# Kernel tuning notes

Hardware: AMD Instinct MI355X
Metric: run time of the kernel (lower is better)

The kernel has to match this reference:

```python
import jax, jax.numpy as jnp
import numpy as np

EPS = 1e-5
N_CAMERAS, N_POINTS = 6, 4


def _bilinear_sample(feats, gx, gy):
    # feats: [B, C, H, W]; gx, gy: [B, Q] in [-1, 1]; align_corners=False, zero padding
    B, C, H, W = feats.shape
    ix = ((gx + 1.0) * W - 1.0) * 0.5
    iy = ((gy + 1.0) * H - 1.0) * 0.5
    x0 = jnp.floor(ix)
    y0 = jnp.floor(iy)
    fx = ix - x0
    fy = iy - y0
    x0i = x0.astype(jnp.int32)
    y0i = y0.astype(jnp.int32)
    ff = feats.reshape(B, C, H * W)

    def corner(xi, yi, w):
        valid = (xi >= 0) & (xi < W) & (yi >= 0) & (yi < H)
        idx = jnp.clip(yi, 0, H - 1) * W + jnp.clip(xi, 0, W - 1)
        v = jnp.take_along_axis(ff, idx[:, None, :], axis=2)  # [B, C, Q]
        return v * (w * valid)[:, None, :]

    return (corner(x0i, y0i, (1 - fx) * (1 - fy))
            + corner(x0i + 1, y0i, fx * (1 - fy))
            + corner(x0i, y0i + 1, (1 - fx) * fy)
            + corner(x0i + 1, y0i + 1, fx * fy))


def setup_inputs() -> dict:
    key = jax.random.key(0)
    ks = jax.random.split(key, 8)
    Hb = Wb = 128
    nq = Hb * Wb
    bs, hidden, N, P = 2, 256, N_CAMERAS, N_POINTS
    C, Hf, Wf = 256, 28, 50

    rho = jnp.broadcast_to((jnp.arange(Hb, dtype=jnp.float32) / Hb)[:, None], (Hb, Wb))
    phi = jnp.broadcast_to((jnp.arange(Wb, dtype=jnp.float32) / Wb)[None, :], (Hb, Wb))
    pc_range = jnp.array([51.2, 2.0 * np.pi, -5.0, 3.0], jnp.float32)
    intervals = jnp.array([51.2 / Hb, 2.0 * np.pi / Wb], jnp.float32)
    img_size = jnp.array([1600.0, 900.0], jnp.float32)

    # realistic pinhole lidar->image matrices for 6 surround cameras
    K = np.array([[1200.0, 0, 800, 0], [0, 1200.0, 450, 0], [0, 0, 1, 0], [0, 0, 0, 1]], np.float32)
    mats = []
    for i in range(N):
        yaw = 2.0 * np.pi * i / N
        c, s = np.cos(yaw), np.sin(yaw)
        R = np.array([[s, -c, 0], [0, 0, -1], [c, s, 0]], np.float32)  # x_right, y_down, z_forward
        E = np.eye(4, dtype=np.float32)
        E[:3, :3] = R
        E[:3, 3] = np.array([0.0, 1.5, 0.5], np.float32)
        mats.append(K @ E)
    lidar2imgs = jnp.asarray(np.broadcast_to(np.stack(mats), (bs, N, 4, 4)).copy())

    return {
        'query': jax.random.normal(ks[0], (nq, bs, hidden), jnp.float32),
        'query_pos': jax.random.normal(ks[1], (nq, bs, hidden), jnp.float32),
        'rho': rho,
        'phi': phi,
        'zz_cord': jax.random.uniform(ks[2], (bs, nq, 1), jnp.float32),
        'img_feats': jax.random.normal(ks[3], (bs, N, C, Hf, Wf), jnp.float32),
        'lidar2imgs': lidar2imgs,
        'intervals': intervals,
        'pc_range': pc_range,
        'img_size': img_size,
        'Wa': jax.random.normal(ks[4], (hidden, N * P), jnp.float32) * 0.02,
        'ba': jnp.zeros((N * P,), jnp.float32),
        'Wo': jax.random.normal(ks[5], (hidden, hidden), jnp.float32) * 0.02,
        'bo': jnp.zeros((hidden,), jnp.float32),
    }


def reference(query, query_pos, rho, phi, zz_cord, img_feats, lidar2imgs,
              intervals, pc_range, img_size, Wa, ba, Wo, bo):
    q = jnp.transpose(query + query_pos, (1, 0, 2))  # [bs, nq, h]
    bs, nq, _ = q.shape
    aw = (q @ Wa + ba).reshape(bs, 1, nq, N_CAMERAS, N_POINTS)

    # polar BEV -> cartesian lidar coords
    r = rho.reshape(-1, 1) * pc_range[0] + intervals[0] / 2  # [nq, 1]
    p = phi.reshape(-1, 1) * pc_range[1] - jnp.pi + intervals[1] / 2
    xx = r * jnp.cos(p)
    yy = r * jnp.sin(p)
    zz = zz_cord * (pc_range[3] - pc_range[2]) + pc_range[2]  # [bs, nq, 1]
    xyz = jnp.concatenate([
        jnp.broadcast_to(xx[None], (bs, nq, 1)),
        jnp.broadcast_to(yy[None], (bs, nq, 1)),
        zz,
        jnp.ones((bs, nq, 1), q.dtype),
    ], axis=-1)  # [bs, nq, 4]

    cam = jnp.einsum('bnij,bqj->bnqi', lidar2imgs, xyz)  # [bs, N, nq, 4]
    zc = cam[..., 2]
    gx = cam[..., 0] / jnp.maximum(zc, EPS) / img_size[0]
    gy = cam[..., 1] / jnp.maximum(zc, EPS) / img_size[1]
    gx = (gx - 0.5) * 2.0
    gy = (gy - 0.5) * 2.0
    mask = (zc > EPS) & (gx > -1.0) & (gx < 1.0) & (gy > -1.0) & (gy < 1.0)  # [bs, N, nq]

    B, N, C, H, W = img_feats.shape
    sampled = _bilinear_sample(img_feats.reshape(B * N, C, H, W),
                               gx.reshape(B * N, nq), gy.reshape(B * N, nq))
    sampled = jnp.nan_to_num(sampled.reshape(B, N, C, nq).transpose(0, 2, 3, 1))  # [bs, C, nq, N]

    maskf = mask.transpose(0, 2, 1)[:, None, :, :, None].astype(q.dtype)  # [bs,1,nq,N,1]
    ws = (jax.nn.sigmoid(aw) * maskf).sum(-1)  # [bs, 1, nq, N]
    out = jnp.einsum('bcqn,bqn->bcq', sampled, ws[:, 0])  # [bs, C, nq]
    out = out.transpose(2, 0, 1) @ Wo + bo + query  # dropout p=0 -> identity
    mask_out = mask.transpose(0, 2, 1)[:, None, :, :, None]  # [bs,1,nq,N,1] bool
    return out, mask_out
```

## Files before the change

kernel.cpp:

```cpp
#include <hip/hip_runtime.h>
#include <math.h>

#define NQ    16384
#define BS    2
#define HID   256
#define NCAM  6
#define NPTS  4
#define CF    256
#define HF    28
#define WF    50
#define HWF   (HF*WF)
#define NIMG  (BS*NCAM)
#define EPSV  1e-5f
#define GQ    16

typedef __attribute__((ext_vector_type(8))) short short8v;
typedef __attribute__((ext_vector_type(4))) float float4v;

__device__ __forceinline__ unsigned short f2bf(float f) {
    unsigned u = __float_as_uint(f);
    u += 0x7fffu + ((u >> 16) & 1u);
    return (unsigned short)(u >> 16);
}
__device__ __forceinline__ float bfLO(unsigned u) { return __uint_as_float(u << 16); }
__device__ __forceinline__ float bfHI(unsigned u) { return __uint_as_float(u & 0xffff0000u); }

__global__ __launch_bounds__(256) void transpose_feats(
    const float* __restrict__ feats, unsigned short* __restrict__ featsT)
{
    __shared__ float tile[32][33];
    const int img = blockIdx.x / 44;
    const int hw0 = (blockIdx.x % 44) * 32;
    const int tx = threadIdx.x & 31;
    const int ty = threadIdx.x >> 5;
    for (int ct = 0; ct < 8; ++ct) {
        const int c0 = ct * 32;
        #pragma unroll
        for (int i = 0; i < 4; ++i) {
            const int c  = c0 + ty + 8 * i;
            const int hw = hw0 + tx;
            tile[ty + 8 * i][tx] = (hw < HWF) ? feats[((size_t)img * CF + c) * HWF + hw] : 0.f;
        }
        __syncthreads();
        #pragma unroll
        for (int i = 0; i < 4; ++i) {
            const int hw = hw0 + ty + 8 * i;
            if (hw < HWF)
                featsT[((size_t)img * HWF + hw) * CF + c0 + tx] = f2bf(tile[tx][ty + 8 * i]);
        }
        __syncthreads();
    }
}

__global__ __launch_bounds__(256) void transpose_wo_wa(
    const float* __restrict__ Wo, const float* __restrict__ Wa,
    unsigned short* __restrict__ WoT, unsigned short* __restrict__ WaT)
{
    if (blockIdx.x < 64) {
        __shared__ float tile[32][33];
        const int kt = blockIdx.x >> 3, nt = blockIdx.x & 7;
        const int tx = threadIdx.x & 31;
        const int ty = threadIdx.x >> 5;
        #pragma unroll
        for (int i = 0; i < 4; ++i)
            tile[ty + 8 * i][tx] = Wo[(size_t)(kt * 32 + ty + 8 * i) * HID + nt * 32 + tx];
        __syncthreads();
        #pragma unroll
        for (int i = 0; i < 4; ++i)
            WoT[(size_t)(nt * 32 + ty + 8 * i) * HID + kt * 32 + tx] = f2bf(tile[tx][ty + 8 * i]);
    } else {
        #pragma unroll
        for (int v = 0; v < 4; ++v) {
            const int idx = (blockIdx.x - 64) * 1024 + v * 256 + threadIdx.x;
            const int j = idx >> 8, k = idx & 255;
            WaT[idx] = (j < 24) ? f2bf(Wa[k * 24 + j]) : (unsigned short)0;
        }
    }
}

__global__ __launch_bounds__(512) void ca_fused3(
    const float* __restrict__ query, const float* __restrict__ query_pos,
    const float* __restrict__ rho,   const float* __restrict__ phi,
    const float* __restrict__ zz,    const unsigned short* __restrict__ featsT,
    const float* __restrict__ l2i,   const float* __restrict__ intervals,
    const float* __restrict__ pc_range, const float* __restrict__ img_size,
    const unsigned short* __restrict__ WaT, const float* __restrict__ ba,
    const unsigned short* __restrict__ WoT, const float* __restrict__ bo,
    float* __restrict__ out)
{
    __shared__ char  fab[GQ * 512];
    __shared__ float awl[GQ][36];

    const int tid  = threadIdx.x;
    const int wave = tid >> 6;
    const int lane = tid & 63;
    const int l32  = lane & 31;
    const int r    = wave * 2 + (lane >> 5);
    const int base = blockIdx.x * GQ;
    const int g    = base + r;
    const int b    = g >> 14;
    const int q    = g & (NQ - 1);
    const size_t qrow = ((size_t)q * BS + b) * HID;

    {
        const float4 a0 = *reinterpret_cast<const float4*>(&query[qrow + 8 * l32]);
        const float4 a1 = *reinterpret_cast<const float4*>(&query[qrow + 8 * l32 + 4]);
        const float4 p0 = *reinterpret_cast<const float4*>(&query_pos[qrow + 8 * l32]);
        const float4 p1 = *reinterpret_cast<const float4*>(&query_pos[qrow + 8 * l32 + 4]);
        uint4 u;
        u.x = ((unsigned)f2bf(a0.y + p0.y) << 16) | f2bf(a0.x + p0.x);
        u.y = ((unsigned)f2bf(a0.w + p0.w) << 16) | f2bf(a0.z + p0.z);
        u.z = ((unsigned)f2bf(a1.y + p1.y) << 16) | f2bf(a1.x + p1.x);
        u.w = ((unsigned)f2bf(a1.w + p1.w) << 16) | f2bf(a1.z + p1.z);
        *reinterpret_cast<uint4*>(fab + ((unsigned)(r * 512 + 16 * l32) ^ ((unsigned)(r & 7) << 4))) = u;
    }

    float gxs[NCAM], gys[NCAM];
    bool  msk[NCAM];
    {
        const float pc0 = pc_range[0], pc1 = pc_range[1];
        const float pc2 = pc_range[2], pc3 = pc_range[3];
        const float rr = rho[q] * pc0 + intervals[0] * 0.5f;
        const float pp = phi[q] * pc1 - 3.14159265358979323846f + intervals[1] * 0.5f;
        const float xx = rr * cosf(pp);
        const float yy = rr * sinf(pp);
        const float z  = zz[b * NQ + q] * (pc3 - pc2) + pc2;
        const float iw = img_size[0], ih = img_size[1];
        #pragma unroll
        for (int n = 0; n < NCAM; ++n) {
            const float* M = l2i + (b * NCAM + n) * 16;
            const float cx = M[0]*xx + M[1]*yy + M[2]*z  + M[3];
            const float cy = M[4]*xx + M[5]*yy + M[6]*z  + M[7];
            const float cz = M[8]*xx + M[9]*yy + M[10]*z + M[11];
            const float d  = fmaxf(cz, EPSV);
            const float gx = (cx / d / iw - 0.5f) * 2.0f;
            const float gy = (cy / d / ih - 0.5f) * 2.0f;
            msk[n] = (cz > EPSV) && (gx > -1.0f) && (gx < 1.0f)
                                 && (gy > -1.0f) && (gy < 1.0f);
            gxs[n] = gx; gys[n] = gy;
        }
    }
    if (l32 < NCAM)
        out[(size_t)NQ * BS * HID + ((size_t)b * NQ + q) * NCAM + l32] =
            msk[l32] ? 1.0f : 0.0f;

    __syncthreads();

    if (wave < 2) {
        const int arow = lane & 15;
        const int g4   = lane >> 4;
        float4v aw = {0.f, 0.f, 0.f, 0.f};
        #pragma unroll
        for (int kk = 0; kk < 8; ++kk) {
            const int k0 = kk * 32 + g4 * 8;
            const short8v af = *reinterpret_cast<const short8v*>(
                fab + ((unsigned)(arow * 512 + k0 * 2) ^ ((unsigned)(arow & 7) << 4)));
            const short8v bw = *reinterpret_cast<const short8v*>(
                WaT + (size_t)(wave * 16 + arow) * HID + k0);
            aw = __builtin_amdgcn_mfma_f32_16x16x32_bf16(af, bw, aw, 0, 0, 0);
        }
        #pragma unroll
        for (int i = 0; i < 4; ++i)
            awl[g4 * 4 + i][wave * 16 + arow] = aw[i];
    }
    __syncthreads();

    float wsv[NCAM];
    {
        float sv = 0.f;
        if (l32 < 24) {
            const float x = awl[r][l32] + ba[l32];
            sv = 1.0f / (1.0f + __expf(-x));
        }
        sv += __shfl_xor(sv, 1);
        sv += __shfl_xor(sv, 2);
        #pragma unroll
        for (int n = 0; n < NCAM; ++n)
            wsv[n] = __shfl(sv, (lane & 32) + 4 * n);
    }

    float acc[8] = {0.f, 0.f, 0.f, 0.f, 0.f, 0.f, 0.f, 0.f};
    for (int n = 0; n < NCAM; ++n) {
        if (msk[n]) {
            const float ixf = ((gxs[n] + 1.0f) * WF - 1.0f) * 0.5f;
            const float iyf = ((gys[n] + 1.0f) * HF - 1.0f) * 0.5f;
            const float x0f = floorf(ixf), y0f = floorf(iyf);
            const float fx = ixf - x0f, fy = iyf - y0f;
            const int x0 = (int)x0f, y0 = (int)y0f;
            const int   xs[4] = {x0, x0 + 1, x0,     x0 + 1};
            const int   ys[4] = {y0, y0,     y0 + 1, y0 + 1};
            const float wc[4] = {(1.f-fx)*(1.f-fy), fx*(1.f-fy),
                                 (1.f-fx)*fy,       fx*fy};
            const unsigned short* fb = featsT + (size_t)(b * NCAM + n) * HWF * CF + 8 * l32;
            #pragma unroll
            for (int c4 = 0; c4 < 4; ++c4) {
                const bool v = (xs[c4] >= 0) && (xs[c4] < WF) &&
                               (ys[c4] >= 0) && (ys[c4] < HF);
                const int xc = min(max(xs[c4], 0), WF - 1);
                const int yc = min(max(ys[c4], 0), HF - 1);
                const float wnv = wsv[n] * (v ? wc[c4] : 0.0f);
                const uint4 u = *reinterpret_cast<const uint4*>(fb + (size_t)(yc * WF + xc) * CF);
                acc[0] += wnv * bfLO(u.x); acc[1] += wnv * bfHI(u.x);
                acc[2] += wnv * bfLO(u.y); acc[3] += wnv * bfHI(u.y);
                acc[4] += wnv * bfLO(u.z); acc[5] += wnv * bfHI(u.z);
                acc[6] += wnv * bfLO(u.w); acc[7] += wnv * bfHI(u.w);
            }
        }
    }

    {
        uint4 u;
        u.x = ((unsigned)f2bf(acc[1]) << 16) | f2bf(acc[0]);
        u.y = ((unsigned)f2bf(acc[3]) << 16) | f2bf(acc[2]);
        u.z = ((unsigned)f2bf(acc[5]) << 16) | f2bf(acc[4]);
        u.w = ((unsigned)f2bf(acc[7]) << 16) | f2bf(acc[6]);
        *reinterpret_cast<uint4*>(fab + ((unsigned)(r * 512 + 16 * l32) ^ ((unsigned)(r & 7) << 4))) = u;
    }
    __syncthreads();

    const int colw = lane & 15;
    const int g4   = lane >> 4;
    #pragma unroll
    for (int t = 0; t < 2; ++t) {
        const int col = wave * 16 + t * 128 + colw;
        float4v dacc = {0.f, 0.f, 0.f, 0.f};
        #pragma unroll
        for (int kk = 0; kk < 8; ++kk) {
            const int k0 = kk * 32 + g4 * 8;
            const short8v af = *reinterpret_cast<const short8v*>(
                fab + ((unsigned)(colw * 512 + k0 * 2) ^ ((unsigned)(colw & 7) << 4)));
            const short8v bw = *reinterpret_cast<const short8v*>(
                WoT + (size_t)col * HID + k0);
            dacc = __builtin_amdgcn_mfma_f32_16x16x32_bf16(af, bw, dacc, 0, 0, 0);
        }
        #pragma unroll
        for (int rg = 0; rg < 4; ++rg) {
            const int rowq = g4 * 4 + rg;
            const int gq = base + rowq;
            const int bq = gq >> 14, qq = gq & (NQ - 1);
            const size_t addr = ((size_t)qq * BS + bq) * HID + col;
            out[addr] = dacc[rg] + bo[col] + query[addr];
        }
    }
}

#define CHUNK 32
__global__ __launch_bounds__(512, 2) void ca_fused_fb(
    const float* __restrict__ query, const float* __restrict__ query_pos,
    const float* __restrict__ rho, const float* __restrict__ phi,
    const float* __restrict__ zz, const float* __restrict__ feats,
    const float* __restrict__ l2i, const float* __restrict__ intervals,
    const float* __restrict__ pc_range, const float* __restrict__ img_size,
    const float* __restrict__ Wa, const float* __restrict__ ba,
    const float* __restrict__ Wo, const float* __restrict__ bo,
    float* __restrict__ out)
{
    __shared__ float fa[8][HID];
    __shared__ float wolds[CHUNK][HID];
    const int tid  = threadIdx.x;
    const int wave = tid >> 6;
    const int lane = tid & 63;
    const int g    = blockIdx.x * 8 + wave;
    const int b    = g / NQ;
    const int q    = g - b * NQ;
    const size_t qrow = ((size_t)q * BS + b) * HID;
    {
        float qv[4];
        #pragma unroll
        for (int k = 0; k < 4; ++k) {
            const int h = lane + 64 * k;
            qv[k] = query[qrow + h] + query_pos[qrow + h];
        }
        const float pc0 = pc_range[0], pc1 = pc_range[1];
        const float pc2 = pc_range[2], pc3 = pc_range[3];
        const float r = rho[q] * pc0 + intervals[0] * 0.5f;
        const float p = phi[q] * pc1 - 3.14159265358979323846f + intervals[1] * 0.5f;
        const float xx = r * cosf(p);
        const float yy = r * sinf(p);
        const float z  = zz[b * NQ + q] * (pc3 - pc2) + pc2;
        const float iw = img_size[0], ih = img_size[1];
        float gxs[NCAM], gys[NCAM], wss[NCAM];
        bool  msk[NCAM];
        #pragma unroll
        for (int n = 0; n < NCAM; ++n) {
            const float* M = l2i + (b * NCAM + n) * 16;
            const float cx = M[0]*xx + M[1]*yy + M[2]*z  + M[3];
            const float cy = M[4]*xx + M[5]*yy + M[6]*z  + M[7];
            const float cz = M[8]*xx + M[9]*yy + M[10]*z + M[11];
            const float d  = fmaxf(cz, EPSV);
            const float gx = (cx / d / iw - 0.5f) * 2.0f;
            const float gy = (cy / d / ih - 0.5f) * 2.0f;
            msk[n] = (cz > EPSV) && (gx > -1.0f) && (gx < 1.0f)
                                 && (gy > -1.0f) && (gy < 1.0f);
            gxs[n] = gx; gys[n] = gy; wss[n] = 0.0f;
        }
        for (int n = 0; n < NCAM; ++n) {
            if (!msk[n]) continue;
            float s = 0.0f;
            #pragma unroll
            for (int pp = 0; pp < NPTS; ++pp) {
                const int j = n * NPTS + pp;
                float part = 0.0f;
                #pragma unroll
                for (int k = 0; k < 4; ++k)
                    part += qv[k] * Wa[(lane + 64 * k) * 24 + j];
                #pragma unroll
                for (int off = 32; off; off >>= 1)
                    part += __shfl_xor(part, off, 64);
                s += 1.0f / (1.0f + expf(-(part + ba[j])));
            }
            wss[n] = s;
        }
        if (lane < NCAM)
            out[(size_t)NQ * BS * HID + ((size_t)b * NQ + q) * NCAM + lane] =
                msk[lane] ? 1.0f : 0.0f;
        float acc[4] = {0.f, 0.f, 0.f, 0.f};
        for (int n = 0; n < NCAM; ++n) {
            if (!msk[n]) continue;
            const float ixf = ((gxs[n] + 1.0f) * WF - 1.0f) * 0.5f;
            const float iyf = ((gys[n] + 1.0f) * HF - 1.0f) * 0.5f;
            const float x0f = floorf(ixf), y0f = floorf(iyf);
            const float fx = ixf - x0f, fy = iyf - y0f;
            const int x0 = (int)x0f, y0 = (int)y0f;
            const int   xs[4] = {x0, x0 + 1, x0,     x0 + 1};
            const int   ys[4] = {y0, y0,     y0 + 1, y0 + 1};
            const float wc[4] = {(1.f-fx)*(1.f-fy), fx*(1.f-fy),
                                 (1.f-fx)*fy,       fx*fy};
            int   offc[4];
            float wv[4];
            #pragma unroll
            for (int c4 = 0; c4 < 4; ++c4) {
                const bool v = (xs[c4] >= 0) && (xs[c4] < WF) &&
                               (ys[c4] >= 0) && (ys[c4] < HF);
                const int xc = min(max(xs[c4], 0), WF - 1);
                const int yc = min(max(ys[c4], 0), HF - 1);
                offc[c4] = yc * WF + xc;
                wv[c4]   = v ? wc[c4] : 0.0f;
            }
            const float wn = wss[n];
            const float* fbp = feats + (size_t)(b * NCAM + n) * CF * HWF;
            #pragma unroll
            for (int k = 0; k < 4; ++k) {
                const float* fc = fbp + (size_t)(lane + 64 * k) * HWF;
                const float sv = wv[0]*fc[offc[0]] + wv[1]*fc[offc[1]]
                               + wv[2]*fc[offc[2]] + wv[3]*fc[offc[3]];
                acc[k] += wn * sv;
            }
        }
        #pragma unroll
        for (int k = 0; k < 4; ++k)
            fa[wave][lane + 64 * k] = acc[k];
    }
    float racc[4] = {0.f, 0.f, 0.f, 0.f};
    const int h0 = 4 * lane;
    for (int c0 = 0; c0 < HID; c0 += CHUNK) {
        __syncthreads();
        for (int i = tid; i < CHUNK * HID; i += 512)
            wolds[i >> 8][i & 255] = Wo[(size_t)(c0 + (i >> 8)) * HID + (i & 255)];
        __syncthreads();
        #pragma unroll 8
        for (int c = 0; c < CHUNK; ++c) {
            const float fav = fa[wave][c0 + c];
            const float4 wv4 = *reinterpret_cast<const float4*>(&wolds[c][h0]);
            racc[0] += fav * wv4.x;
            racc[1] += fav * wv4.y;
            racc[2] += fav * wv4.z;
            racc[3] += fav * wv4.w;
        }
    }
    float4 o;
    o.x = racc[0] + bo[h0 + 0] + query[qrow + h0 + 0];
    o.y = racc[1] + bo[h0 + 1] + query[qrow + h0 + 1];
    o.z = racc[2] + bo[h0 + 2] + query[qrow + h0 + 2];
    o.w = racc[3] + bo[h0 + 3] + query[qrow + h0 + 3];
    *reinterpret_cast<float4*>(&out[qrow + h0]) = o;
}

extern "C" void kernel_launch(void* const* d_in, const int* in_sizes, int n_in,
                              void* d_out, int out_size, void* d_ws, size_t ws_size,
                              hipStream_t stream) {
    const float* query     = (const float*)d_in[0];
    const float* query_pos = (const float*)d_in[1];
    const float* rho       = (const float*)d_in[2];
    const float* phi       = (const float*)d_in[3];
    const float* zz        = (const float*)d_in[4];
    const float* feats     = (const float*)d_in[5];
    const float* l2i       = (const float*)d_in[6];
    const float* intervals = (const float*)d_in[7];
    const float* pc_range  = (const float*)d_in[8];
    const float* img_size  = (const float*)d_in[9];
    const float* Wa        = (const float*)d_in[10];
    const float* ba        = (const float*)d_in[11];
    const float* Wo        = (const float*)d_in[12];
    const float* bo        = (const float*)d_in[13];
    float* out = (float*)d_out;

    const size_t featsT_bytes = (size_t)NIMG * HWF * CF * 2;
    const size_t woT_bytes    = (size_t)HID * HID * 2;
    const size_t waT_bytes    = (size_t)32 * HID * 2;
    const size_t need = featsT_bytes + woT_bytes + waT_bytes;

    if (ws_size >= need) {
        unsigned short* featsT = (unsigned short*)d_ws;
        unsigned short* WoT    = (unsigned short*)((char*)d_ws + featsT_bytes);
        unsigned short* WaT    = (unsigned short*)((char*)d_ws + featsT_bytes + woT_bytes);
        transpose_feats<<<NIMG * 44, 256, 0, stream>>>(feats, featsT);
        transpose_wo_wa<<<72, 256, 0, stream>>>(Wo, Wa, WoT, WaT);
        ca_fused3<<<(BS * NQ) / GQ, 512, 0, stream>>>(query, query_pos, rho, phi, zz,
                                                      featsT, l2i, intervals, pc_range,
                                                      img_size, WaT, ba, WoT, bo, out);
    } else {
        ca_fused_fb<<<(BS * NQ) / 8, 512, 0, stream>>>(query, query_pos, rho, phi, zz,
                                                       feats, l2i, intervals, pc_range,
                                                       img_size, Wa, ba, Wo, bo, out);
    }
}
```

Measured before the change: 79.48 us.

## Merge prep kernels and restructure fused kernel to one query per wave

Merges the two preprocessing transpose kernels into a single launch. The main kernel now handles 8 queries per block with one wave per query. The feature gathers for all cameras are issued up front, independent of the attention-weight GEMM, with clamped coordinates instead of per-camera mask branches. Each wave computes the attention-weight MFMA itself and uses shuffles instead of an LDS round trip and an extra barrier. The trade-off is doubled blocks, half of the 16-row MFMA tiles wasted on padding, and gathers for masked cameras that are loaded but then zero-weighted.

Measured after the change: 215.3 us. 2.71x slower.

```diff
diff --git a/kernel.cpp b/kernel.cpp
--- a/kernel.cpp
+++ b/kernel.cpp
@@ -12,7 +12,7 @@
 #define HWF   (HF*WF)
 #define NIMG  (BS*NCAM)
 #define EPSV  1e-5f
-#define GQ    16
+#define GQ    8
 
 typedef __attribute__((ext_vector_type(8))) short short8v;
 typedef __attribute__((ext_vector_type(4))) float float4v;
@@ -25,42 +25,37 @@
 __device__ __forceinline__ float bfLO(unsigned u) { return __uint_as_float(u << 16); }
 __device__ __forceinline__ float bfHI(unsigned u) { return __uint_as_float(u & 0xffff0000u); }
 
-__global__ __launch_bounds__(256) void transpose_feats(
-    const float* __restrict__ feats, unsigned short* __restrict__ featsT)
+__global__ __launch_bounds__(256) void prep_all(
+    const float* __restrict__ feats, const float* __restrict__ Wo,
+    const float* __restrict__ Wa, unsigned short* __restrict__ featsT,
+    unsigned short* __restrict__ WoT, unsigned short* __restrict__ WaT)
 {
     __shared__ float tile[32][33];
-    const int img = blockIdx.x / 44;
-    const int hw0 = (blockIdx.x % 44) * 32;
     const int tx = threadIdx.x & 31;
     const int ty = threadIdx.x >> 5;
-    for (int ct = 0; ct < 8; ++ct) {
-        const int c0 = ct * 32;
-        #pragma unroll
-        for (int i = 0; i < 4; ++i) {
-            const int c  = c0 + ty + 8 * i;
-            const int hw = hw0 + tx;
-            tile[ty + 8 * i][tx] = (hw < HWF) ? feats[((size_t)img * CF + c) * HWF + hw] : 0.f;
-        }
-        __syncthreads();
-        #pragma unroll
-        for (int i = 0; i < 4; ++i) {
-            const int hw = hw0 + ty + 8 * i;
-            if (hw < HWF)
-                featsT[((size_t)img * HWF + hw) * CF + c0 + tx] = f2bf(tile[tx][ty + 8 * i]);
-        }
-        __syncthreads();
-    }
-}
-
-__global__ __launch_bounds__(256) void transpose_wo_wa(
-    const float* __restrict__ Wo, const float* __restrict__ Wa,
-    unsigned short* __restrict__ WoT, unsigned short* __restrict__ WaT)
-{
-    if (blockIdx.x < 64) {
-        __shared__ float tile[32][33];
-        const int kt = blockIdx.x >> 3, nt = blockIdx.x & 7;
-        const int tx = threadIdx.x & 31;
-        const int ty = threadIdx.x >> 5;
+    if (blockIdx.x < 528) {
+        const int img = blockIdx.x / 44;
+        const int hw0 = (blockIdx.x % 44) * 32;
+        for (int ct = 0; ct < 8; ++ct) {
+            const int c0 = ct * 32;
+            #pragma unroll
+            for (int i = 0; i < 4; ++i) {
+                const int c  = c0 + ty + 8 * i;
+                const int hw = hw0 + tx;
+                tile[ty + 8 * i][tx] = (hw < HWF) ? feats[((size_t)img * CF + c) * HWF + hw] : 0.f;
+            }
+            __syncthreads();
+            #pragma unroll
+            for (int i = 0; i < 4; ++i) {
+                const int hw = hw0 + ty + 8 * i;
+                if (hw < HWF)
+                    featsT[((size_t)img * HWF + hw) * CF + c0 + tx] = f2bf(tile[tx][ty + 8 * i]);
+            }
+            __syncthreads();
+        }
+    } else if (blockIdx.x < 592) {
+        const int bid = blockIdx.x - 528;
+        const int kt = bid >> 3, nt = bid & 7;
         #pragma unroll
         for (int i = 0; i < 4; ++i)
             tile[ty + 8 * i][tx] = Wo[(size_t)(kt * 32 + ty + 8 * i) * HID + nt * 32 + tx];
@@ -69,16 +64,17 @@
         for (int i = 0; i < 4; ++i)
             WoT[(size_t)(nt * 32 + ty + 8 * i) * HID + kt * 32 + tx] = f2bf(tile[tx][ty + 8 * i]);
     } else {
+        const int bid = blockIdx.x - 592;
         #pragma unroll
         for (int v = 0; v < 4; ++v) {
-            const int idx = (blockIdx.x - 64) * 1024 + v * 256 + threadIdx.x;
+            const int idx = bid * 1024 + v * 256 + threadIdx.x;
             const int j = idx >> 8, k = idx & 255;
             WaT[idx] = (j < 24) ? f2bf(Wa[k * 24 + j]) : (unsigned short)0;
         }
     }
 }
 
-__global__ __launch_bounds__(512) void ca_fused3(
+__global__ __launch_bounds__(512) void ca_fused4(
     const float* __restrict__ query, const float* __restrict__ query_pos,
     const float* __restrict__ rho,   const float* __restrict__ phi,
     const float* __restrict__ zz,    const unsigned short* __restrict__ featsT,
@@ -88,14 +84,13 @@
     const unsigned short* __restrict__ WoT, const float* __restrict__ bo,
     float* __restrict__ out)
 {
-    __shared__ char  fab[GQ * 512];
-    __shared__ float awl[GQ][36];
+    __shared__ char fabq[16 * 512];
+    __shared__ char fabf[16 * 512];
 
     const int tid  = threadIdx.x;
     const int wave = tid >> 6;
     const int lane = tid & 63;
-    const int l32  = lane & 31;
-    const int r    = wave * 2 + (lane >> 5);
+    const int r    = wave;
     const int base = blockIdx.x * GQ;
     const int g    = base + r;
     const int b    = g >> 14;
@@ -103,20 +98,17 @@
     const size_t qrow = ((size_t)q * BS + b) * HID;
 
     {
-        const float4 a0 = *reinterpret_cast<const float4*>(&query[qrow + 8 * l32]);
-        const float4 a1 = *reinterpret_cast<const float4*>(&query[qrow + 8 * l32 + 4]);
-        const float4 p0 = *reinterpret_cast<const float4*>(&query_pos[qrow + 8 * l32]);
-        const float4 p1 = *reinterpret_cast<const float4*>(&query_pos[qrow + 8 * l32 + 4]);
-        uint4 u;
-        u.x = ((unsigned)f2bf(a0.y + p0.y) << 16) | f2bf(a0.x + p0.x);
-        u.y = ((unsigned)f2bf(a0.w + p0.w) << 16) | f2bf(a0.z + p0.z);
-        u.z = ((unsigned)f2bf(a1.y + p1.y) << 16) | f2bf(a1.x + p1.x);
-        u.w = ((unsigned)f2bf(a1.w + p1.w) << 16) | f2bf(a1.z + p1.z);
-        *reinterpret_cast<uint4*>(fab + ((unsigned)(r * 512 + 16 * l32) ^ ((unsigned)(r & 7) << 4))) = u;
-    }
-
+        const float4 qa = *reinterpret_cast<const float4*>(&query[qrow + 4 * lane]);
+        const float4 qp = *reinterpret_cast<const float4*>(&query_pos[qrow + 4 * lane]);
+        uint2 u;
+        u.x = ((unsigned)f2bf(qa.y + qp.y) << 16) | f2bf(qa.x + qp.x);
+        u.y = ((unsigned)f2bf(qa.w + qp.w) << 16) | f2bf(qa.z + qp.z);
+        *reinterpret_cast<uint2*>(fabq + ((unsigned)(r * 512 + 8 * lane) ^ ((unsigned)(r & 7) << 4))) = u;
+    }
+    __syncthreads();
+
+    bool msk[NCAM];
     float gxs[NCAM], gys[NCAM];
-    bool  msk[NCAM];
     {
         const float pc0 = pc_range[0], pc1 = pc_range[1];
         const float pc2 = pc_range[2], pc3 = pc_range[3];
@@ -140,106 +132,119 @@
             gxs[n] = gx; gys[n] = gy;
         }
     }
-    if (l32 < NCAM)
-        out[(size_t)NQ * BS * HID + ((size_t)b * NQ + q) * NCAM + l32] =
-            msk[l32] ? 1.0f : 0.0f;
-
+    {
+        unsigned mbits = 0;
+        #pragma unroll
+        for (int n = 0; n < NCAM; ++n) mbits |= (msk[n] ? 1u : 0u) << n;
+        if (lane < NCAM)
+            out[(size_t)NQ * BS * HID + ((size_t)b * NQ + q) * NCAM + lane] =
+                ((mbits >> lane) & 1u) ? 1.0f : 0.0f;
+    }
+
+    float inner[NCAM][4];
+    #pragma unroll
+    for (int n = 0; n < NCAM; ++n) {
+        float ixf = ((gxs[n] + 1.0f) * WF - 1.0f) * 0.5f;
+        float iyf = ((gys[n] + 1.0f) * HF - 1.0f) * 0.5f;
+        ixf = fminf(fmaxf(ixf, -8.0f), 56.0f);
+        iyf = fminf(fmaxf(iyf, -8.0f), 34.0f);
+        const float x0f = floorf(ixf), y0f = floorf(iyf);
+        const float fx = ixf - x0f, fy = iyf - y0f;
+        const int x0 = (int)x0f, y0 = (int)y0f;
+        const int   xs[4] = {x0, x0 + 1, x0,     x0 + 1};
+        const int   ys[4] = {y0, y0,     y0 + 1, y0 + 1};
+        const float wc[4] = {(1.f-fx)*(1.f-fy), fx*(1.f-fy),
+                             (1.f-fx)*fy,       fx*fy};
+        const unsigned short* fb = featsT + (size_t)(b * NCAM + n) * HWF * CF + 4 * lane;
+        inner[n][0] = inner[n][1] = inner[n][2] = inner[n][3] = 0.f;
+        #pragma unroll
+        for (int c4 = 0; c4 < 4; ++c4) {
+            const bool v = (xs[c4] >= 0) && (xs[c4] < WF) &&
+                           (ys[c4] >= 0) && (ys[c4] < HF);
+            const int xc = min(max(xs[c4], 0), WF - 1);
+            const int yc = min(max(ys[c4], 0), HF - 1);
+            const float w = v ? wc[c4] : 0.0f;
+            const uint2 u = *reinterpret_cast<const uint2*>(fb + (size_t)(yc * WF + xc) * CF);
+            inner[n][0] += w * bfLO(u.x); inner[n][1] += w * bfHI(u.x);
+            inner[n][2] += w * bfLO(u.y); inner[n][3] += w * bfHI(u.y);
+        }
+    }
+
+    const int arow = lane & 15;
+    const int g4   = lane >> 4;
+    float4v aw0 = {0.f, 0.f, 0.f, 0.f}, aw1 = {0.f, 0.f, 0.f, 0.f};
+    #pragma unroll
+    for (int kk = 0; kk < 8; ++kk) {
+        const int k0 = kk * 32 + g4 * 8;
+        const short8v af = *reinterpret_cast<const short8v*>(
+            fabq + ((unsigned)(arow * 512 + k0 * 2) ^ ((unsigned)(arow & 7) << 4)));
+        const short8v b0 = *reinterpret_cast<const short8v*>(WaT + (size_t)arow * HID + k0);
+        const short8v b1 = *reinterpret_cast<const short8v*>(WaT + (size_t)(16 + arow) * HID + k0);
+        aw0 = __builtin_amdgcn_mfma_f32_16x16x32_bf16(af, b0, aw0, 0, 0, 0);
+        aw1 = __builtin_amdgcn_mfma_f32_16x16x32_bf16(af, b1, aw1, 0, 0, 0);
+    }
+
+    float wsv[NCAM];
+    {
+        const int rm = r & 3;
+        const float v0 = rm == 0 ? aw0[0] : rm == 1 ? aw0[1] : rm == 2 ? aw0[2] : aw0[3];
+        const float v1 = rm == 0 ? aw1[0] : rm == 1 ? aw1[1] : rm == 2 ? aw1[2] : aw1[3];
+        const int j = lane & 31;
+        const int srcl = 16 * (r >> 2) + (j & 15);
+        const float s0 = __shfl(v0, srcl);
+        const float s1 = __shfl(v1, srcl);
+        const float val = (j < 16) ? s0 : s1;
+        float s = 0.f;
+        if (j < 24) s = 1.0f / (1.0f + __expf(-(val + ba[j])));
+        s += __shfl_xor(s, 1);
+        s += __shfl_xor(s, 2);
+        #pragma unroll
+        for (int n = 0; n < NCAM; ++n)
+            wsv[n] = msk[n] ? __shfl(s, 4 * n) : 0.f;
+    }
+
+    float acc[4] = {0.f, 0.f, 0.f, 0.f};
+    #pragma unroll
+    for (int n = 0; n < NCAM; ++n) {
+        acc[0] += wsv[n] * inner[n][0];
+        acc[1] += wsv[n] * inner[n][1];
+        acc[2] += wsv[n] * inner[n][2];
+        acc[3] += wsv[n] * inner[n][3];
+    }
+
+    {
+        uint2 u;
+        u.x = ((unsigned)f2bf(acc[1]) << 16) | f2bf(acc[0]);
+        u.y = ((unsigned)f2bf(acc[3]) << 16) | f2bf(acc[2]);
+        *reinterpret_cast<uint2*>(fabf + ((unsigned)(r * 512 + 8 * lane) ^ ((unsigned)(r & 7) << 4))) = u;
+    }
     __syncthreads();
 
-    if (wave < 2) {
-        const int arow = lane & 15;
-        const int g4   = lane >> 4;
-        float4v aw = {0.f, 0.f, 0.f, 0.f};
+    {
+        float4v d0 = {0.f, 0.f, 0.f, 0.f}, d1 = {0.f, 0.f, 0.f, 0.f};
+        const int col0 = wave * 32 + arow;
+        const int col1 = col0 + 16;
         #pragma unroll
         for (int kk = 0; kk < 8; ++kk) {
             const int k0 = kk * 32 + g4 * 8;
             const short8v af = *reinterpret_cast<const short8v*>(
-                fab + ((unsigned)(arow * 512 + k0 * 2) ^ ((unsigned)(arow & 7) << 4)));
-            const short8v bw = *reinterpret_cast<const short8v*>(
-                WaT + (size_t)(wave * 16 + arow) * HID + k0);
-            aw = __builtin_amdgcn_mfma_f32_16x16x32_bf16(af, bw, aw, 0, 0, 0);
-        }
-        #pragma unroll
-        for (int i = 0; i < 4; ++i)
-            awl[g4 * 4 + i][wave * 16 + arow] = aw[i];
-    }
-    __syncthreads();
-
-    float wsv[NCAM];
-    {
-        float sv = 0.f;
-        if (l32 < 24) {
-            const float x = awl[r][l32] + ba[l32];
-            sv = 1.0f / (1.0f + __expf(-x));
-        }
-        sv += __shfl_xor(sv, 1);
-        sv += __shfl_xor(sv, 2);
-        #pragma unroll
-        for (int n = 0; n < NCAM; ++n)
-            wsv[n] = __shfl(sv, (lane & 32) + 4 * n);
-    }
-
-    float acc[8] = {0.f, 0.f, 0.f, 0.f, 0.f, 0.f, 0.f, 0.f};
-    for (int n = 0; n < NCAM; ++n) {
-        if (msk[n]) {
-            const float ixf = ((gxs[n] + 1.0f) * WF - 1.0f) * 0.5f;
-            const float iyf = ((gys[n] + 1.0f) * HF - 1.0f) * 0.5f;
-            const float x0f = floorf(ixf), y0f = floorf(iyf);
-            const float fx = ixf - x0f, fy = iyf - y0f;
-            const int x0 = (int)x0f, y0 = (int)y0f;
-            const int   xs[4] = {x0, x0 + 1, x0,     x0 + 1};
-            const int   ys[4] = {y0, y0,     y0 + 1, y0 + 1};
-            const float wc[4] = {(1.f-fx)*(1.f-fy), fx*(1.f-fy),
-                                 (1.f-fx)*fy,       fx*fy};
-            const unsigned short* fb = featsT + (size_t)(b * NCAM + n) * HWF * CF + 8 * l32;
-            #pragma unroll
-            for (int c4 = 0; c4 < 4; ++c4) {
-                const bool v = (xs[c4] >= 0) && (xs[c4] < WF) &&
-                               (ys[c4] >= 0) && (ys[c4] < HF);
-                const int xc = min(max(xs[c4], 0), WF - 1);
-                const int yc = min(max(ys[c4], 0), HF - 1);
-                const float wnv = wsv[n] * (v ? wc[c4] : 0.0f);
-                const uint4 u = *reinterpret_cast<const uint4*>(fb + (size_t)(yc * WF + xc) * CF);
-                acc[0] += wnv * bfLO(u.x); acc[1] += wnv * bfHI(u.x);
-                acc[2] += wnv * bfLO(u.y); acc[3] += wnv * bfHI(u.y);
-                acc[4] += wnv * bfLO(u.z); acc[5] += wnv * bfHI(u.z);
-                acc[6] += wnv * bfLO(u.w); acc[7] += wnv * bfHI(u.w);
-            }
-        }
-    }
-
-    {
-        uint4 u;
-        u.x = ((unsigned)f2bf(acc[1]) << 16) | f2bf(acc[0]);
-        u.y = ((unsigned)f2bf(acc[3]) << 16) | f2bf(acc[2]);
-        u.z = ((unsigned)f2bf(acc[5]) << 16) | f2bf(acc[4]);
-        u.w = ((unsigned)f2bf(acc[7]) << 16) | f2bf(acc[6]);
-        *reinterpret_cast<uint4*>(fab + ((unsigned)(r * 512 + 16 * l32) ^ ((unsigned)(r & 7) << 4))) = u;
-    }
-    __syncthreads();
-
-    const int colw = lane & 15;
-    const int g4   = lane >> 4;
-    #pragma unroll
-    for (int t = 0; t < 2; ++t) {
-        const int col = wave * 16 + t * 128 + colw;
-        float4v dacc = {0.f, 0.f, 0.f, 0.f};
-        #pragma unroll
-        for (int kk = 0; kk < 8; ++kk) {
-            const int k0 = kk * 32 + g4 * 8;
-            const short8v af = *reinterpret_cast<const short8v*>(
-                fab + ((unsigned)(colw * 512 + k0 * 2) ^ ((unsigned)(colw & 7) << 4)));
-            const short8v bw = *reinterpret_cast<const short8v*>(
-                WoT + (size_t)col * HID + k0);
-            dacc = __builtin_amdgcn_mfma_f32_16x16x32_bf16(af, bw, dacc, 0, 0, 0);
-        }
-        #pragma unroll
-        for (int rg = 0; rg < 4; ++rg) {
-            const int rowq = g4 * 4 + rg;
-            const int gq = base + rowq;
-            const int bq = gq >> 14, qq = gq & (NQ - 1);
-            const size_t addr = ((size_t)qq * BS + bq) * HID + col;
-            out[addr] = dacc[rg] + bo[col] + query[addr];
+                fabf + ((unsigned)(arow * 512 + k0 * 2) ^ ((unsigned)(arow & 7) << 4)));
+            const short8v b0 = *reinterpret_cast<const short8v*>(WoT + (size_t)col0 * HID + k0);
+            const short8v b1 = *reinterpret_cast<const short8v*>(WoT + (size_t)col1 * HID + k0);
+            d0 = __builtin_amdgcn_mfma_f32_16x16x32_bf16(af, b0, d0, 0, 0, 0);
+            d1 = __builtin_amdgcn_mfma_f32_16x16x32_bf16(af, b1, d1, 0, 0, 0);
+        }
+        if (g4 < 2) {
+            #pragma unroll
+            for (int rg = 0; rg < 4; ++rg) {
+                const int row = g4 * 4 + rg;
+                const int gq = base + row;
+                const int bq = gq >> 14, qq = gq & (NQ - 1);
+                const size_t a0 = ((size_t)qq * BS + bq) * HID + col0;
+                const size_t a1 = ((size_t)qq * BS + bq) * HID + col1;
+                out[a0] = d0[rg] + bo[col0] + query[a0];
+                out[a1] = d1[rg] + bo[col1] + query[a1];
+            }
         }
     }
 }
@@ -404,9 +409,8 @@
         unsigned short* featsT = (unsigned short*)d_ws;
         unsigned short* WoT    = (unsigned short*)((char*)d_ws + featsT_bytes);
         unsigned short* WaT    = (unsigned short*)((char*)d_ws + featsT_bytes + woT_bytes);
-        transpose_feats<<<NIMG * 44, 256, 0, stream>>>(feats, featsT);
-        transpose_wo_wa<<<72, 256, 0, stream>>>(Wo, Wa, WoT, WaT);
-        ca_fused3<<<(BS * NQ) / GQ, 512, 0, stream>>>(query, query_pos, rho, phi, zz,
+        prep_all<<<600, 256, 0, stream>>>(feats, Wo, Wa, featsT, WoT, WaT);
+        ca_fused4<<<(BS * NQ) / GQ, 512, 0, stream>>>(query, query_pos, rho, phi, zz,
                                                       featsT, l2i, intervals, pc_range,
                                                       img_size, WaT, ba, WoT, bo, out);
     } else {
```
